# Kernel optimization log

Hardware: AMD Instinct MI355X
Metric: run time of the kernel (lower is better)

## Reference

```python
import jax, jax.numpy as jnp
import numpy as np

HEADS = 4
DIM_HEAD = 32


def setup_inputs() -> dict:
    key = jax.random.key(0)
    k1, k2, k3 = jax.random.split(key, 3)
    B, L, D = 16, 8192, 256
    hidden = HEADS * DIM_HEAD  # 128
    x = jax.random.normal(k1, (B, L, D), dtype=jnp.float32)
    W_qkv = jax.random.normal(k2, (D, 3 * hidden), dtype=jnp.float32) * (D ** -0.5)
    W_out = jax.random.normal(k3, (hidden, D), dtype=jnp.float32) * (hidden ** -0.5)
    b_out = jnp.zeros((D,), dtype=jnp.float32)
    return {"x": x, "W_qkv": W_qkv, "W_out": W_out, "b_out": b_out}


def reference(x, W_qkv, W_out, b_out):
    B, L, D = x.shape
    scale = DIM_HEAD ** -0.5
    # 1x1 conv == per-token matmul
    qkv = jnp.einsum('bld,df->blf', x, W_qkv)  # [B, L, 3*h*dh]
    qkv = qkv.reshape(B, L, 3, HEADS, DIM_HEAD)
    q = jnp.transpose(qkv[:, :, 0], (0, 2, 1, 3)) * scale          # [B, h, L, d]
    k = jax.nn.softmax(jnp.transpose(qkv[:, :, 1], (0, 2, 1, 3)), axis=2)  # softmax over L
    v = jnp.transpose(qkv[:, :, 2], (0, 2, 1, 3))                  # [B, h, L, e]
    context = jnp.einsum('bhld,bhle->bhde', k, v)                  # [B, h, d, e]
    out = jnp.einsum('bhde,bhld->bhle', context, q)                # [B, h, L, e]
    out = jnp.transpose(out, (0, 2, 1, 3)).reshape(B, L, HEADS * DIM_HEAD)
    return jnp.einsum('blf,fd->bld', out, W_out) + b_out
```

## Files before the change

kernel.cpp:

```cpp
#include <hip/hip_runtime.h>
#include <math.h>


#define BL 131072

typedef __attribute__((ext_vector_type(8))) short bf16x8;
typedef __attribute__((ext_vector_type(4))) float f32x4;

__device__ __forceinline__ ushort bf16_rn(float f) {
    unsigned u = __float_as_uint(f);
    return (ushort)((u + 0x7FFFu + ((u >> 16) & 1u)) >> 16);
}
__device__ __forceinline__ float bf16f(ushort h) { return __uint_as_float(((unsigned)h) << 16); }

__device__ __forceinline__ void glds16(const void* g, void* l) {
    __builtin_amdgcn_global_load_lds((const __attribute__((address_space(1))) unsigned int*)g,
                                     (__attribute__((address_space(3))) unsigned int*)l,
                                     16, 0, 0);
}

__global__ __launch_bounds__(256) void init_stats(float* S, float* Z) {
    int i = blockIdx.x * 256 + threadIdx.x;
    if (i < 65536) S[i] = 0.f;
    if (i < 2048) Z[i] = 0.f;
}

__global__ __launch_bounds__(256) void convert_w(const float* __restrict__ W,
                                                 ushort* __restrict__ wh,
                                                 ushort* __restrict__ wl) {
    int n = blockIdx.x, k = threadIdx.x;
    float f = W[k * 384 + n];
    ushort h = bf16_rn(f);
    wh[n * 256 + k] = h;
    wl[n * 256 + k] = bf16_rn(f - bf16f(h));
}

__global__ __launch_bounds__(256) void gemm1_kernel(
    const float* __restrict__ X,
    const ushort* __restrict__ Wh, const ushort* __restrict__ Wl,
    ushort* __restrict__ Qh, ushort* __restrict__ Ql,
    float* __restrict__ KV) {
    __shared__ __align__(16) float  As[4096];
    __shared__ __align__(16) ushort Bsh[4096];
    __shared__ __align__(16) ushort Bsl[4096];
    const int tid = threadIdx.x;
    const int col0 = blockIdx.x * 128;
    const int row0 = blockIdx.y * 128;
    const int lane = tid & 63, wave = tid >> 6;
    const int wr = (wave & 1) * 64, wc = (wave >> 1) * 64;
    const int m = lane & 15, quad = lane >> 4;
    const int ra = lane >> 3, pa = lane & 7;
    const int rb = lane >> 2, pb = lane & 3;

    f32x4 acc[4][4] = {};

    for (int k0 = 0; k0 < 256; k0 += 32) {
#pragma unroll
        for (int s = 0; s < 4; ++s) {
            int seg = s * 4 + wave;
            int r = seg * 8 + ra;
            int q = pa ^ (r & 7);
            glds16(&X[(long)(row0 + r) * 256 + k0 + q * 4], &As[seg * 256]);
        }
#pragma unroll
        for (int s = 0; s < 2; ++s) {
            int seg = s * 4 + wave;
            int r = seg * 16 + rb;
            int q = pb ^ ((r >> 1) & 3);
            glds16(&Wh[(long)(col0 + r) * 256 + k0 + q * 8], &Bsh[seg * 512]);
            glds16(&Wl[(long)(col0 + r) * 256 + k0 + q * 8], &Bsl[seg * 512]);
        }
        __syncthreads();

        bf16x8 bh[4], bl[4];
#pragma unroll
        for (int i = 0; i < 4; ++i) {
            int r = wc + i * 16 + m;
            int p = quad ^ ((r >> 1) & 3);
            bh[i] = *(const bf16x8*)&Bsh[r * 32 + p * 8];
            bl[i] = *(const bf16x8*)&Bsl[r * 32 + p * 8];
        }
#pragma unroll
        for (int i = 0; i < 4; ++i) {
            int r = wr + i * 16 + m;
            int p0 = (quad * 2) ^ (r & 7);
            int p1 = (quad * 2 + 1) ^ (r & 7);
            f32x4 a0 = *(const f32x4*)&As[r * 32 + p0 * 4];
            f32x4 a1 = *(const f32x4*)&As[r * 32 + p1 * 4];
            float f[8] = {a0[0], a0[1], a0[2], a0[3], a1[0], a1[1], a1[2], a1[3]};
            bf16x8 ah, al;
#pragma unroll
            for (int e = 0; e < 8; ++e) {
                ushort h = bf16_rn(f[e]);
                ah[e] = (short)h;
                al[e] = (short)bf16_rn(f[e] - bf16f(h));
            }
#pragma unroll
            for (int j = 0; j < 4; ++j) {
                acc[i][j] = __builtin_amdgcn_mfma_f32_16x16x32_bf16(ah, bh[j], acc[i][j], 0, 0, 0);
                acc[i][j] = __builtin_amdgcn_mfma_f32_16x16x32_bf16(ah, bl[j], acc[i][j], 0, 0, 0);
                acc[i][j] = __builtin_amdgcn_mfma_f32_16x16x32_bf16(al, bh[j], acc[i][j], 0, 0, 0);
            }
        }
        __syncthreads();
    }

    if (blockIdx.x == 0) {
#pragma unroll
        for (int i = 0; i < 4; ++i)
#pragma unroll
            for (int r4 = 0; r4 < 4; ++r4) {
                long row = row0 + wr + i * 16 + quad * 4 + r4;
#pragma unroll
                for (int j = 0; j < 4; ++j) {
                    float v = acc[i][j][r4];
                    int col = wc + j * 16 + m;
                    ushort h = bf16_rn(v);
                    Qh[row * 128 + col] = h;
                    Ql[row * 128 + col] = bf16_rn(v - bf16f(h));
                }
            }
    } else {
        int vofs = (blockIdx.x == 2) ? 32 : 0;
#pragma unroll
        for (int i = 0; i < 4; ++i)
#pragma unroll
            for (int r4 = 0; r4 < 4; ++r4) {
                long row = row0 + wr + i * 16 + quad * 4 + r4;
                long b = row >> 13, l = row & 8191;
#pragma unroll
                for (int j = 0; j < 4; ++j) {
                    int c = wc + j * 16 + m;
                    int h = c >> 5, dd = c & 31;
                    KV[(((b * 4 + h) * 8192 + l) * 64) + vofs + dd] = acc[i][j][r4];
                }
            }
    }
}

__global__ __launch_bounds__(256) void ksum_hb(const float* __restrict__ KV,
                                               float* __restrict__ S,
                                               float* __restrict__ Z) {
    int bx = blockIdx.x;
    int c = bx & 7, bh = bx >> 3;
    const float* slab = KV + ((long)bh * 8192 + c * 1024) * 64;
    __shared__ float tile[64][68];
    const int tid = threadIdx.x;
    const int dcol = tid & 31;
    const int e0 = (tid >> 5) * 4;
    const int c4 = tid & 15, lrow = tid >> 4;
    float z = 0.f;
    f32x4 acc = {0.f, 0.f, 0.f, 0.f};

    for (int t0 = 0; t0 < 1024; t0 += 64) {
#pragma unroll
        for (int u = 0; u < 4; ++u) {
            int l = u * 16 + lrow;
            float4 w = *(const float4*)&slab[((long)(t0 + l)) * 64 + c4 * 4];
            if (c4 < 8) { w.x = expf(w.x); w.y = expf(w.y); w.z = expf(w.z); w.w = expf(w.w); }
            *(float4*)&tile[l][c4 * 4] = w;
        }
        __syncthreads();
#pragma unroll 8
        for (int l = 0; l < 64; ++l) {
            float e = tile[l][dcol];
            f32x4 vv = *(const f32x4*)&tile[l][32 + e0];
            z += e;
            acc[0] += e * vv[0]; acc[1] += e * vv[1];
            acc[2] += e * vv[2]; acc[3] += e * vv[3];
        }
        __syncthreads();
    }
    if (tid < 32) atomicAdd(&Z[bh * 32 + dcol], z);
#pragma unroll
    for (int j = 0; j < 4; ++j)
        atomicAdd(&S[((long)bh * 32 + dcol) * 32 + e0 + j], acc[j]);
}

__global__ __launch_bounds__(256) void combine_kernel(const float* __restrict__ S,
                                                      const float* __restrict__ Z,
                                                      const float* __restrict__ Wout,
                                                      ushort* __restrict__ m2h,
                                                      ushort* __restrict__ m2l) {
    int bh = blockIdx.x;
    int b = bh >> 2, h = bh & 3;
    int n = threadIdx.x;
    __shared__ float ctx[32][32];
    __shared__ float zs[32];
    if (n < 32) zs[n] = Z[bh * 32 + n];
    __syncthreads();
#pragma unroll
    for (int t = 0; t < 4; ++t) {
        int idx = t * 256 + n;
        int d = idx >> 5, e = idx & 31;
        ctx[d][e] = S[(long)bh * 1024 + idx] / zs[d];
    }
    __syncthreads();
    const float scale = 0.17677669529663687f;
    float acc[32];
#pragma unroll
    for (int d = 0; d < 32; ++d) acc[d] = 0.f;
    for (int e = 0; e < 32; ++e) {
        float w = Wout[(h * 32 + e) * 256 + n];
#pragma unroll
        for (int d = 0; d < 32; ++d) acc[d] += ctx[d][e] * w;
    }
#pragma unroll
    for (int d = 0; d < 32; ++d) {
        float v = acc[d] * scale;
        long idx = ((long)(b * 256 + n)) * 128 + h * 32 + d;
        ushort hh = bf16_rn(v);
        m2h[idx] = hh;
        m2l[idx] = bf16_rn(v - bf16f(hh));
    }
}

__global__ __launch_bounds__(256) void gemm2_kernel(
    const ushort* __restrict__ Ahp, const ushort* __restrict__ Alp,
    const ushort* __restrict__ Bhp, const ushort* __restrict__ Blp,
    const float* __restrict__ bias, float* __restrict__ out) {
    __shared__ __align__(16) ushort Ash[4096];
    __shared__ __align__(16) ushort Asl[4096];
    __shared__ __align__(16) ushort Bsh[4096];
    __shared__ __align__(16) ushort Bsl[4096];
    const int tid = threadIdx.x;
    const int col0 = blockIdx.x * 128;
    const int row0 = blockIdx.y * 128;
    const long bz = blockIdx.z;
    const ushort* Ah = Ahp + bz * (8192L * 128);
    const ushort* Al = Alp + bz * (8192L * 128);
    const ushort* Bh = Bhp + bz * (256L * 128);
    const ushort* Bl = Blp + bz * (256L * 128);
    const int lane = tid & 63, wave = tid >> 6;
    const int wr = (wave & 1) * 64, wc = (wave >> 1) * 64;
    const int m = lane & 15, quad = lane >> 4;
    const int rb = lane >> 2, pb = lane & 3;

    f32x4 acc[4][4] = {};

    for (int k0 = 0; k0 < 128; k0 += 32) {
#pragma unroll
        for (int s = 0; s < 2; ++s) {
            int seg = s * 4 + wave;
            int r = seg * 16 + rb;
            int q = pb ^ ((r >> 1) & 3);
            glds16(&Ah[(long)(row0 + r) * 128 + k0 + q * 8], &Ash[seg * 512]);
            glds16(&Al[(long)(row0 + r) * 128 + k0 + q * 8], &Asl[seg * 512]);
            glds16(&Bh[(long)(col0 + r) * 128 + k0 + q * 8], &Bsh[seg * 512]);
            glds16(&Bl[(long)(col0 + r) * 128 + k0 + q * 8], &Bsl[seg * 512]);
        }
        __syncthreads();

        bf16x8 af[2][4], bg[2][4];
#pragma unroll
        for (int i = 0; i < 4; ++i) {
            int rA = wr + i * 16 + m;
            int pA = quad ^ ((rA >> 1) & 3);
            af[0][i] = *(const bf16x8*)&Ash[rA * 32 + pA * 8];
            af[1][i] = *(const bf16x8*)&Asl[rA * 32 + pA * 8];
            int rB = wc + i * 16 + m;
            int pB = quad ^ ((rB >> 1) & 3);
            bg[0][i] = *(const bf16x8*)&Bsh[rB * 32 + pB * 8];
            bg[1][i] = *(const bf16x8*)&Bsl[rB * 32 + pB * 8];
        }
#pragma unroll
        for (int i = 0; i < 4; ++i)
#pragma unroll
            for (int j = 0; j < 4; ++j) {
                acc[i][j] = __builtin_amdgcn_mfma_f32_16x16x32_bf16(af[0][i], bg[0][j], acc[i][j], 0, 0, 0);
                acc[i][j] = __builtin_amdgcn_mfma_f32_16x16x32_bf16(af[0][i], bg[1][j], acc[i][j], 0, 0, 0);
                acc[i][j] = __builtin_amdgcn_mfma_f32_16x16x32_bf16(af[1][i], bg[0][j], acc[i][j], 0, 0, 0);
            }
        __syncthreads();
    }

    float bv[4];
#pragma unroll
    for (int j = 0; j < 4; ++j) bv[j] = bias[col0 + wc + j * 16 + m];
    float* outb = out + bz * (8192L * 256);
#pragma unroll
    for (int i = 0; i < 4; ++i)
#pragma unroll
        for (int r4 = 0; r4 < 4; ++r4) {
            long row = row0 + wr + i * 16 + quad * 4 + r4;
#pragma unroll
            for (int j = 0; j < 4; ++j)
                outb[row * 256 + col0 + wc + j * 16 + m] = acc[i][j][r4] + bv[j];
        }
}

extern "C" void kernel_launch(void* const* d_in, const int* in_sizes, int n_in,
                              void* d_out, int out_size, void* d_ws, size_t ws_size,
                              hipStream_t stream) {
    const float* x     = (const float*)d_in[0];
    const float* W_qkv = (const float*)d_in[1];
    const float* W_out = (const float*)d_in[2];
    const float* b_out = (const float*)d_in[3];
    float* out = (float*)d_out;

    char* p = (char*)d_ws;
    float* kv   = (float*)p;  p += (long)64 * 8192 * 64 * 4;
    float* S    = (float*)p;  p += 65536 * 4;
    float* Z    = (float*)p;  p += 2048 * 4;
    ushort* wth = (ushort*)p; p += 384 * 256 * 2;
    ushort* wtl = (ushort*)p; p += 384 * 256 * 2;
    ushort* qh  = (ushort*)p; p += (long)BL * 128 * 2;
    ushort* ql  = (ushort*)p; p += (long)BL * 128 * 2;
    ushort* m2h = (ushort*)p; p += 16 * 256 * 128 * 2;
    ushort* m2l = (ushort*)p; p += 16 * 256 * 128 * 2;

    init_stats<<<264, 256, 0, stream>>>(S, Z);
    convert_w<<<384, 256, 0, stream>>>(W_qkv, wth, wtl);

    gemm1_kernel<<<dim3(3, 1024), 256, 0, stream>>>(x, wth, wtl, qh, ql, kv);

    ksum_hb<<<512, 256, 0, stream>>>(kv, S, Z);
    combine_kernel<<<64, 256, 0, stream>>>(S, Z, W_out, m2h, m2l);

    gemm2_kernel<<<dim3(2, 64, 16), 256, 0, stream>>>(qh, ql, m2h, m2l, b_out, out);
}
```

Baseline: 437.3 us.

## Use packed bf16 convert, XCD-aware block mapping, and fast exp

Replaces the software bf16 rounding with the hardware v_cvt_pk_bf16_f32 instruction, which packs two conversions into one in the gemm1 split-precision inner loop. It also flattens the gemm1 grid and remaps block indices so that the three column blocks sharing an X row tile are scheduled on the same XCD, which should improve L2 reuse of X. ksum switches from expf to __expf. The fast exp and the hardware rounding may differ slightly in accuracy from the originals.

New measurement: 431.3 us. About the same (-1.4%).

```diff
diff --git a/kernel.cpp b/kernel.cpp
--- a/kernel.cpp
+++ b/kernel.cpp
@@ -6,10 +6,15 @@
 
 typedef __attribute__((ext_vector_type(8))) short bf16x8;
 typedef __attribute__((ext_vector_type(4))) float f32x4;
-
+typedef __attribute__((ext_vector_type(4))) unsigned u32x4;
+
+__device__ __forceinline__ unsigned cvt_pk2(float a, float b) {
+    unsigned r;
+    asm("v_cvt_pk_bf16_f32 %0, %1, %2" : "=v"(r) : "v"(a), "v"(b));
+    return r;
+}
 __device__ __forceinline__ ushort bf16_rn(float f) {
-    unsigned u = __float_as_uint(f);
-    return (ushort)((u + 0x7FFFu + ((u >> 16) & 1u)) >> 16);
+    return (ushort)cvt_pk2(f, f);
 }
 __device__ __forceinline__ float bf16f(ushort h) { return __uint_as_float(((unsigned)h) << 16); }
 
@@ -44,8 +49,13 @@
     __shared__ __align__(16) ushort Bsh[4096];
     __shared__ __align__(16) ushort Bsl[4096];
     const int tid = threadIdx.x;
-    const int col0 = blockIdx.x * 128;
-    const int row0 = blockIdx.y * 128;
+    const int wg = blockIdx.x;
+    const int xcd = wg & 7;
+    const int slot = wg >> 3;
+    const int cb = slot % 3;
+    const int yb = (slot / 3) * 8 + xcd;
+    const int col0 = cb * 128;
+    const int row0 = yb * 128;
     const int lane = tid & 63, wave = tid >> 6;
     const int wr = (wave & 1) * 64, wc = (wave >> 1) * 64;
     const int m = lane & 15, quad = lane >> 4;
@@ -87,14 +97,25 @@
             int p1 = (quad * 2 + 1) ^ (r & 7);
             f32x4 a0 = *(const f32x4*)&As[r * 32 + p0 * 4];
             f32x4 a1 = *(const f32x4*)&As[r * 32 + p1 * 4];
-            float f[8] = {a0[0], a0[1], a0[2], a0[3], a1[0], a1[1], a1[2], a1[3]};
-            bf16x8 ah, al;
-#pragma unroll
-            for (int e = 0; e < 8; ++e) {
-                ushort h = bf16_rn(f[e]);
-                ah[e] = (short)h;
-                al[e] = (short)bf16_rn(f[e] - bf16f(h));
-            }
+            u32x4 ahw, alw;
+#pragma unroll
+            for (int e = 0; e < 2; ++e) {
+                float f0 = a0[2 * e], f1 = a0[2 * e + 1];
+                unsigned h = cvt_pk2(f0, f1);
+                ahw[e] = h;
+                alw[e] = cvt_pk2(f0 - __uint_as_float(h << 16),
+                                 f1 - __uint_as_float(h & 0xFFFF0000u));
+            }
+#pragma unroll
+            for (int e = 0; e < 2; ++e) {
+                float f0 = a1[2 * e], f1 = a1[2 * e + 1];
+                unsigned h = cvt_pk2(f0, f1);
+                ahw[2 + e] = h;
+                alw[2 + e] = cvt_pk2(f0 - __uint_as_float(h << 16),
+                                     f1 - __uint_as_float(h & 0xFFFF0000u));
+            }
+            bf16x8 ah = __builtin_bit_cast(bf16x8, ahw);
+            bf16x8 al = __builtin_bit_cast(bf16x8, alw);
 #pragma unroll
             for (int j = 0; j < 4; ++j) {
                 acc[i][j] = __builtin_amdgcn_mfma_f32_16x16x32_bf16(ah, bh[j], acc[i][j], 0, 0, 0);
@@ -105,7 +126,7 @@
         __syncthreads();
     }
 
-    if (blockIdx.x == 0) {
+    if (cb == 0) {
 #pragma unroll
         for (int i = 0; i < 4; ++i)
 #pragma unroll
@@ -121,7 +142,7 @@
                 }
             }
     } else {
-        int vofs = (blockIdx.x == 2) ? 32 : 0;
+        int vofs = (cb == 2) ? 32 : 0;
 #pragma unroll
         for (int i = 0; i < 4; ++i)
 #pragma unroll
@@ -157,7 +178,7 @@
         for (int u = 0; u < 4; ++u) {
             int l = u * 16 + lrow;
             float4 w = *(const float4*)&slab[((long)(t0 + l)) * 64 + c4 * 4];
-            if (c4 < 8) { w.x = expf(w.x); w.y = expf(w.y); w.z = expf(w.z); w.w = expf(w.w); }
+            if (c4 < 8) { w.x = __expf(w.x); w.y = __expf(w.y); w.z = __expf(w.z); w.w = __expf(w.w); }
             *(float4*)&tile[l][c4 * 4] = w;
         }
         __syncthreads();
@@ -312,7 +333,7 @@
     init_stats<<<264, 256, 0, stream>>>(S, Z);
     convert_w<<<384, 256, 0, stream>>>(W_qkv, wth, wtl);
 
-    gemm1_kernel<<<dim3(3, 1024), 256, 0, stream>>>(x, wth, wtl, qh, ql, kv);
+    gemm1_kernel<<<3072, 256, 0, stream>>>(x, wth, wtl, qh, ql, kv);
 
     ksum_hb<<<512, 256, 0, stream>>>(kv, S, Z);
     combine_kernel<<<64, 256, 0, stream>>>(S, Z, W_out, m2h, m2l);
```
